# Kernel tuning notes

Hardware: AMD Instinct MI355X
Metric: run time of the kernel (lower is better)

## Reference

```python
import jax, jax.numpy as jnp
import numpy as np

N = 8192      # nodes
C = 128       # node_channels
E = 262144    # edges (avg degree 32)


def _glorot(key, shape):
    lim = 1.0 / np.sqrt(shape[0])
    return jax.random.uniform(key, shape, jnp.float32, -lim, lim)


def setup_inputs() -> dict:
    key = jax.random.key(0)
    ks = jax.random.split(key, 12)
    inp = {
        "x": jax.random.normal(ks[0], (N, C), jnp.float32),
        "edge_index": jax.random.randint(ks[1], (2, E), 0, N, dtype=jnp.int32).astype(jnp.int64),
        # edge encoder: two parallel GCNConv layers producing source/target embeddings
        "Ws": _glorot(ks[2], (C, C)), "bs": jnp.zeros((C,), jnp.float32),
        "Wt": _glorot(ks[3], (C, C)), "bt": jnp.zeros((C,), jnp.float32),
        # NodeModel GCNConv weights (layers used in forward: 1, 2, mu, 5, 6)
        "W1": _glorot(ks[4], (C, C)), "b1": jnp.zeros((C,), jnp.float32),
        "W2": _glorot(ks[5], (C, C)), "b2": jnp.zeros((C,), jnp.float32),
        "Wmu": _glorot(ks[6], (C, C)), "bmu": jnp.zeros((C,), jnp.float32),
        "W5": _glorot(ks[7], (C, C)), "b5": jnp.zeros((C,), jnp.float32),
        "W6": _glorot(ks[8], (C, C)), "b6": jnp.zeros((C,), jnp.float32),
    }
    return inp


def _gcn(x, W, b, src, dst, dis, n):
    """GCNConv: D^-1/2 (A + I) D^-1/2 X W + b, edge flow src -> dst."""
    h = x @ W                                    # [n, C]
    norm = dis[src] * dis[dst]                   # [E]
    agg = jax.ops.segment_sum(h[src] * norm[:, None], dst, num_segments=n)
    agg = agg + h * (dis * dis)[:, None]         # self-loop term
    return agg + b


def reference(x, edge_index, Ws, bs, Wt, bt, W1, b1, W2, b2, Wmu, bmu, W5, b5, W6, b6):
    src, dst = edge_index[0], edge_index[1]
    n = x.shape[0]
    # degree with self-loops (shared by all GCN layers, same graph)
    deg = jax.ops.segment_sum(jnp.ones((src.shape[0],), x.dtype), dst, num_segments=n) + 1.0
    dis = deg ** -0.5

    # edge encoder -> source/target embeddings, dense inner-product decoder (sigmoid=False)
    s = _gcn(x, Ws, bs, src, dst, dis, n)
    t = _gcn(x, Wt, bt, src, dst, dis, n)
    adj_pred = s @ t.T                           # [n, n]

    # NodeModel (eval mode: reparametrize returns mu; logstd branch is dead code)
    h = jax.nn.relu(_gcn(x, W1, b1, src, dst, dis, n))
    h = jax.nn.relu(_gcn(h, W2, b2, src, dst, dis, n))
    h = _gcn(h, Wmu, bmu, src, dst, dis, n)
    h = jax.nn.relu(_gcn(h, W5, b5, src, dst, dis, n))
    h = jax.nn.relu(_gcn(h, W6, b6, src, dst, dis, n))
    return adj_pred, h
```

## Files before the change

### kernel.cpp

```cpp
#include <hip/hip_runtime.h>
#include <hip/hip_bf16.h>

#define CCH 128

typedef __attribute__((ext_vector_type(8))) short s8v;
typedef __attribute__((ext_vector_type(4))) float f4v;

__device__ __forceinline__ unsigned short f2bf(float f){
  unsigned int u = __float_as_uint(f);
  u += 0x7fffu + ((u >> 16) & 1u);
  return (unsigned short)(u >> 16);
}

__global__ void k_deg(const int* __restrict__ dst, int* __restrict__ deg, int e){
  int i = blockIdx.x * blockDim.x + threadIdx.x;
  if (i < e) atomicAdd(&deg[dst[i]], 1);
}

__global__ __launch_bounds__(256) void k_disscale(const int* __restrict__ deg,
    const float* __restrict__ x, float* __restrict__ dis, float* __restrict__ g, int n){
  int t = blockIdx.x * 256 + threadIdx.x;
  int i = t >> 5, c = t & 31;
  if (i >= n) return;
  float di = rsqrtf((float)deg[i] + 1.0f);
  if (c == 0) dis[i] = di;
  float4 v = ((const float4*)x)[(size_t)i * 32 + c];
  v.x *= di; v.y *= di; v.z *= di; v.w *= di;
  ((float4*)g)[(size_t)i * 32 + c] = v;
}

__global__ void k_scan(const int* __restrict__ deg, int* __restrict__ row_ptr,
                       int* __restrict__ cursor, int n){
  __shared__ int part[1024];
  int t = threadIdx.x;
  int base = t * 8;
  int loc[8];
  int s = 0;
  #pragma unroll
  for (int i = 0; i < 8; ++i){ loc[i] = s; s += deg[base + i]; }
  part[t] = s;
  __syncthreads();
  for (int off = 1; off < 1024; off <<= 1){
    int v = (t >= off) ? part[t - off] : 0;
    __syncthreads();
    part[t] += v;
    __syncthreads();
  }
  int prev = t ? part[t - 1] : 0;
  #pragma unroll
  for (int i = 0; i < 8; ++i){
    int v = prev + loc[i];
    row_ptr[base + i] = v;
    cursor[base + i]  = v;
  }
  if (t == 0) row_ptr[n] = part[1023];
}

__global__ void k_scatter(const int* __restrict__ src, const int* __restrict__ dst,
                          int* __restrict__ cursor, int* __restrict__ csr_src, int e){
  int i = blockIdx.x * blockDim.x + threadIdx.x;
  if (i < e){
    int d = dst[i];
    int pos = atomicAdd(&cursor[d], 1);
    csr_src[pos] = src[i];
  }
}

__global__ __launch_bounds__(256) void k_agg(const float* __restrict__ g,
    const int* __restrict__ row_ptr, const int* __restrict__ csr_src,
    float* __restrict__ out, int n){
  int node = (blockIdx.x * blockDim.x + threadIdx.x) >> 6;
  int lane = threadIdx.x & 63;
  if (node >= n) return;
  node = __builtin_amdgcn_readfirstlane(node);
  const float2* g2 = (const float2*)g;
  int st = row_ptr[node], en = row_ptr[node + 1];
  float2 sv = g2[(size_t)node * 64 + lane];
  float ax0 = sv.x, ay0 = sv.y;
  float ax1 = 0.f, ay1 = 0.f, ax2 = 0.f, ay2 = 0.f, ax3 = 0.f, ay3 = 0.f;
  float ax4 = 0.f, ay4 = 0.f, ax5 = 0.f, ay5 = 0.f, ax6 = 0.f, ay6 = 0.f;
  float ax7 = 0.f, ay7 = 0.f;
  int e = st;
  for (; e + 8 <= en; e += 8){
    int s0 = csr_src[e + 0], s1 = csr_src[e + 1], s2 = csr_src[e + 2], s3 = csr_src[e + 3];
    int s4 = csr_src[e + 4], s5 = csr_src[e + 5], s6 = csr_src[e + 6], s7 = csr_src[e + 7];
    float2 v0 = g2[(size_t)s0 * 64 + lane];
    float2 v1 = g2[(size_t)s1 * 64 + lane];
    float2 v2 = g2[(size_t)s2 * 64 + lane];
    float2 v3 = g2[(size_t)s3 * 64 + lane];
    float2 v4 = g2[(size_t)s4 * 64 + lane];
    float2 v5 = g2[(size_t)s5 * 64 + lane];
    float2 v6 = g2[(size_t)s6 * 64 + lane];
    float2 v7 = g2[(size_t)s7 * 64 + lane];
    ax0 += v0.x; ay0 += v0.y;  ax1 += v1.x; ay1 += v1.y;
    ax2 += v2.x; ay2 += v2.y;  ax3 += v3.x; ay3 += v3.y;
    ax4 += v4.x; ay4 += v4.y;  ax5 += v5.x; ay5 += v5.y;
    ax6 += v6.x; ay6 += v6.y;  ax7 += v7.x; ay7 += v7.y;
  }
  for (; e < en; ++e){
    int s = csr_src[e];
    float2 v = g2[(size_t)s * 64 + lane];
    ax0 += v.x; ay0 += v.y;
  }
  float2 o;
  o.x = ((ax0 + ax1) + (ax2 + ax3)) + ((ax4 + ax5) + (ax6 + ax7));
  o.y = ((ay0 + ay1) + (ay2 + ay3)) + ((ay4 + ay5) + (ay6 + ay7));
  ((float2*)out)[(size_t)node * 64 + lane] = o;
}

__global__ __launch_bounds__(256) void k_gemm(const float* __restrict__ A,
    const float* __restrict__ W, const float* __restrict__ bias,
    const float* __restrict__ dis, float* __restrict__ out,
    int relu, int scale_out){
  __shared__ float sW[CCH * CCH];
  __shared__ float sA[16 * CCH];
  int tid = threadIdx.x;
  const float4* W4 = (const float4*)W;
  float4* sW4 = (float4*)sW;
  #pragma unroll
  for (int i = 0; i < 16; ++i) sW4[tid + i * 256] = W4[tid + i * 256];
  int row0 = blockIdx.x * 16;
  const float4* A4 = (const float4*)(A + (size_t)row0 * CCH);
  float4* sA4 = (float4*)sA;
  sA4[tid]       = A4[tid];
  sA4[tid + 256] = A4[tid + 256];
  __syncthreads();

  int r  = tid >> 4;
  int c0 = (tid & 15) << 3;
  float acc[8] = {0.f,0.f,0.f,0.f,0.f,0.f,0.f,0.f};
  #pragma unroll 4
  for (int k = 0; k < CCH; ++k){
    float a = sA[r * CCH + k];
    const float* wr = &sW[k * CCH + c0];
    #pragma unroll
    for (int j = 0; j < 8; ++j) acc[j] += a * wr[j];
  }
  float di = dis[row0 + r];
  size_t g0 = (size_t)(row0 + r) * CCH + c0;
  #pragma unroll
  for (int j = 0; j < 8; ++j){
    float v = fmaf(di, acc[j], bias[c0 + j]);
    if (relu) v = fmaxf(v, 0.f);
    if (scale_out) v *= di;
    out[g0 + j] = v;
  }
}

__global__ void k_tobf16(const float4* __restrict__ a, const float4* __restrict__ b,
                         ushort4* __restrict__ ao, ushort4* __restrict__ bo, int total4){
  int i = blockIdx.x * blockDim.x + threadIdx.x;
  if (i < total4){
    float4 va = a[i];
    float4 vb = b[i];
    ushort4 oa = { f2bf(va.x), f2bf(va.y), f2bf(va.z), f2bf(va.w) };
    ushort4 ob = { f2bf(vb.x), f2bf(vb.y), f2bf(vb.z), f2bf(vb.w) };
    ao[i] = oa;
    bo[i] = ob;
  }
}

__global__ __launch_bounds__(256) void k_adj(const unsigned short* __restrict__ S,
                                             const unsigned short* __restrict__ T,
                                             float* __restrict__ out, int n){
  __shared__ unsigned short sS[128 * 128];
  __shared__ unsigned short sT[128 * 128];
  int tid = threadIdx.x;
  int ntile = n >> 7;
  int tm = blockIdx.x / ntile;
  int tn = blockIdx.x % ntile;

  #pragma unroll
  for (int i = 0; i < 8; ++i){
    int cidx = i * 256 + tid;
    int row = cidx >> 4;
    int o   = cidx & 15;
    int boff = (o * 16) ^ ((row & 7) << 4);
    s8v v = ((const s8v*)(S + (size_t)(tm * 128 + row) * CCH))[o];
    *(s8v*)((char*)sS + row * 256 + boff) = v;
    s8v w = ((const s8v*)(T + (size_t)(tn * 128 + row) * CCH))[o];
    *(s8v*)((char*)sT + row * 256 + boff) = w;
  }
  __syncthreads();

  int lane = tid & 63;
  int w = tid >> 6;
  int wm = (w >> 1) * 64;
  int wn = (w & 1) * 64;

  f4v zero = {0.f, 0.f, 0.f, 0.f};
  f4v acc[4][4];
  #pragma unroll
  for (int a = 0; a < 4; ++a)
    #pragma unroll
    for (int b = 0; b < 4; ++b) acc[a][b] = zero;

  #pragma unroll
  for (int ks = 0; ks < 4; ++ks){
    int boff = ks * 64 + (lane >> 4) * 16;
    s8v af[4], bf[4];
    #pragma unroll
    for (int mi = 0; mi < 4; ++mi){
      int row = wm + mi * 16 + (lane & 15);
      af[mi] = *(const s8v*)((const char*)sS + row * 256 + (boff ^ ((row & 7) << 4)));
    }
    #pragma unroll
    for (int ni = 0; ni < 4; ++ni){
      int row = wn + ni * 16 + (lane & 15);
      bf[ni] = *(const s8v*)((const char*)sT + row * 256 + (boff ^ ((row & 7) << 4)));
    }
    #pragma unroll
    for (int mi = 0; mi < 4; ++mi)
      #pragma unroll
      for (int ni = 0; ni < 4; ++ni)
        acc[mi][ni] = __builtin_amdgcn_mfma_f32_16x16x32_bf16(af[mi], bf[ni], acc[mi][ni], 0, 0, 0);
  }

  int rbase = tm * 128 + wm + (lane >> 4) * 4;
  int cbase = tn * 128 + wn + (lane & 15);
  #pragma unroll
  for (int mi = 0; mi < 4; ++mi)
    #pragma unroll
    for (int ni = 0; ni < 4; ++ni){
      int rr = rbase + mi * 16;
      int cc = cbase + ni * 16;
      #pragma unroll
      for (int r = 0; r < 4; ++r)
        out[(size_t)(rr + r) * n + cc] = acc[mi][ni][r];
    }
}

extern "C" void kernel_launch(void* const* d_in, const int* in_sizes, int n_in,
                              void* d_out, int out_size, void* d_ws, size_t ws_size,
                              hipStream_t stream) {
  const float* x  = (const float*)d_in[0];
  const int*   ei = (const int*)d_in[1];
  const int n = in_sizes[0] / CCH;
  const int e = in_sizes[1] / 2;
  const int* srcv = ei;
  const int* dstv = ei + e;
  const float *Ws  = (const float*)d_in[2],  *bs  = (const float*)d_in[3];
  const float *Wt  = (const float*)d_in[4],  *bt  = (const float*)d_in[5];
  const float *W1  = (const float*)d_in[6],  *b1  = (const float*)d_in[7];
  const float *W2  = (const float*)d_in[8],  *b2  = (const float*)d_in[9];
  const float *Wmu = (const float*)d_in[10], *bmu = (const float*)d_in[11];
  const float *W5  = (const float*)d_in[12], *b5  = (const float*)d_in[13];
  const float *W6  = (const float*)d_in[14], *b6  = (const float*)d_in[15];

  char* ws = (char*)d_ws;
  size_t off = 0;
  auto alloc = [&](size_t bytes) -> void* {
    void* p = ws + off;
    off += (bytes + 255) & ~(size_t)255;
    return p;
  };
  int*   deg     = (int*)alloc((size_t)n * 4);
  float* dis     = (float*)alloc((size_t)n * 4);
  int*   row_ptr = (int*)alloc((size_t)(n + 1) * 4);
  int*   cursor  = (int*)alloc((size_t)n * 4);
  int*   csr_src = (int*)alloc((size_t)e * 4);
  float* g0      = (float*)alloc((size_t)n * CCH * 4);
  float* sumX    = (float*)alloc((size_t)n * CCH * 4);
  float* sbuf    = (float*)alloc((size_t)n * CCH * 4);
  float* tbuf    = (float*)alloc((size_t)n * CCH * 4);
  float* bufA    = (float*)alloc((size_t)n * CCH * 4);
  float* bufB    = (float*)alloc((size_t)n * CCH * 4);
  unsigned short* sb = (unsigned short*)alloc((size_t)n * CCH * 2);
  unsigned short* tb = (unsigned short*)alloc((size_t)n * CCH * 2);

  float* adj  = (float*)d_out;
  float* hout = (float*)d_out + (size_t)n * n;

  hipMemsetAsync(deg, 0, (size_t)n * 4, stream);
  k_deg     <<<(e + 255) / 256, 256, 0, stream>>>(dstv, deg, e);
  k_scan    <<<1, 1024, 0, stream>>>(deg, row_ptr, cursor, n);
  k_disscale<<<(n * 32) / 256, 256, 0, stream>>>(deg, x, dis, g0, n);
  k_scatter <<<(e + 255) / 256, 256, 0, stream>>>(srcv, dstv, cursor, csr_src, e);

  k_agg <<<n / 4, 256, 0, stream>>>(g0, row_ptr, csr_src, sumX, n);
  k_gemm<<<n / 16, 256, 0, stream>>>(sumX, Ws, bs, dis, sbuf, 0, 0);
  k_gemm<<<n / 16, 256, 0, stream>>>(sumX, Wt, bt, dis, tbuf, 0, 0);
  k_gemm<<<n / 16, 256, 0, stream>>>(sumX, W1, b1, dis, bufA, 1, 1);

  k_tobf16<<<((n * CCH / 4) + 255) / 256, 256, 0, stream>>>(
      (const float4*)sbuf, (const float4*)tbuf, (ushort4*)sb, (ushort4*)tb, n * CCH / 4);
  int nt = n / 128;
  k_adj<<<nt * nt, 256, 0, stream>>>(sb, tb, adj, n);

  k_agg <<<n / 4, 256, 0, stream>>>(bufA, row_ptr, csr_src, sumX, n);
  k_gemm<<<n / 16, 256, 0, stream>>>(sumX, W2, b2, dis, bufB, 1, 1);
  k_agg <<<n / 4, 256, 0, stream>>>(bufB, row_ptr, csr_src, sumX, n);
  k_gemm<<<n / 16, 256, 0, stream>>>(sumX, Wmu, bmu, dis, bufA, 0, 1);
  k_agg <<<n / 4, 256, 0, stream>>>(bufA, row_ptr, csr_src, sumX, n);
  k_gemm<<<n / 16, 256, 0, stream>>>(sumX, W5, b5, dis, bufB, 1, 1);
  k_agg <<<n / 4, 256, 0, stream>>>(bufB, row_ptr, csr_src, sumX, n);
  k_gemm<<<n / 16, 256, 0, stream>>>(sumX, W6, b6, dis, hout, 1, 0);
}
```

Baseline: 499.2 us.

## Use split-bf16 MFMA GEMMs, fuse multi-weight GEMM, co-schedule aggregation with adj

Replaces the scalar fp32 128x128 GEMM with an MFMA bf16 kernel that emulates fp32 precision via hi/lo split (three MFMAs per tile), with weights pre-split and transposed once. The aggregation kernel now emits hi/lo bf16 directly, and a single GEMM launch computes the S, T and layer-1 outputs, writing bf16 S/T and removing the separate conversion kernel. The dense adjacency tile kernel is merged with the next layer's aggregation into one launch so the gather work can fill idle CUs alongside the adj GEMM. It trades some precision (split bf16 drops lo*lo terms) and adds weight-split preprocessing.

```diff
diff --git a/kernel.cpp b/kernel.cpp
--- a/kernel.cpp
+++ b/kernel.cpp
@@ -2,6 +2,7 @@
 #include <hip/hip_bf16.h>
 
 #define CCH 128
+#define NADJ 4096
 
 typedef __attribute__((ext_vector_type(8))) short s8v;
 typedef __attribute__((ext_vector_type(4))) float f4v;
@@ -10,6 +11,9 @@
   unsigned int u = __float_as_uint(f);
   u += 0x7fffu + ((u >> 16) & 1u);
   return (unsigned short)(u >> 16);
+}
+__device__ __forceinline__ float bf2f(unsigned short h){
+  return __uint_as_float(((unsigned int)h) << 16);
 }
 
 __global__ void k_deg(const int* __restrict__ dst, int* __restrict__ deg, int e){
@@ -66,13 +70,36 @@
   }
 }
 
-__global__ __launch_bounds__(256) void k_agg(const float* __restrict__ g,
+__global__ __launch_bounds__(256) void k_wsplit(
+    const float* __restrict__ w0, const float* __restrict__ w1, const float* __restrict__ w2,
+    const float* __restrict__ w3, const float* __restrict__ w4, const float* __restrict__ w5,
+    const float* __restrict__ w6,
+    unsigned short* __restrict__ Wth, unsigned short* __restrict__ Wtl){
+  int l = blockIdx.x >> 2;
+  int seg = blockIdx.x & 3;
+  const float* W;
+  switch (l){
+    case 0: W = w0; break; case 1: W = w1; break; case 2: W = w2; break;
+    case 3: W = w3; break; case 4: W = w4; break; case 5: W = w5; break;
+    default: W = w6; break;
+  }
+  unsigned short* oh = Wth + (size_t)l * 16384;
+  unsigned short* ol = Wtl + (size_t)l * 16384;
+  #pragma unroll
+  for (int j = 0; j < 16; ++j){
+    int i = seg * 4096 + j * 256 + threadIdx.x;
+    int nn = i >> 7, kk = i & 127;
+    float v = W[kk * CCH + nn];
+    unsigned short h = f2bf(v);
+    unsigned short lo = f2bf(v - bf2f(h));
+    oh[i] = h;
+    ol[i] = lo;
+  }
+}
+
+__device__ __forceinline__ void agg_body(int node, int lane, const float* __restrict__ g,
     const int* __restrict__ row_ptr, const int* __restrict__ csr_src,
-    float* __restrict__ out, int n){
-  int node = (blockIdx.x * blockDim.x + threadIdx.x) >> 6;
-  int lane = threadIdx.x & 63;
-  if (node >= n) return;
-  node = __builtin_amdgcn_readfirstlane(node);
+    unsigned short* __restrict__ Ahi, unsigned short* __restrict__ Alo){
   const float2* g2 = (const float2*)g;
   int st = row_ptr[node], en = row_ptr[node + 1];
   float2 sv = g2[(size_t)node * 64 + lane];
@@ -102,67 +129,163 @@
     float2 v = g2[(size_t)s * 64 + lane];
     ax0 += v.x; ay0 += v.y;
   }
-  float2 o;
-  o.x = ((ax0 + ax1) + (ax2 + ax3)) + ((ax4 + ax5) + (ax6 + ax7));
-  o.y = ((ay0 + ay1) + (ay2 + ay3)) + ((ay4 + ay5) + (ay6 + ay7));
-  ((float2*)out)[(size_t)node * 64 + lane] = o;
-}
-
-__global__ __launch_bounds__(256) void k_gemm(const float* __restrict__ A,
-    const float* __restrict__ W, const float* __restrict__ bias,
-    const float* __restrict__ dis, float* __restrict__ out,
-    int relu, int scale_out){
-  __shared__ float sW[CCH * CCH];
-  __shared__ float sA[16 * CCH];
+  float ox = ((ax0 + ax1) + (ax2 + ax3)) + ((ax4 + ax5) + (ax6 + ax7));
+  float oy = ((ay0 + ay1) + (ay2 + ay3)) + ((ay4 + ay5) + (ay6 + ay7));
+  unsigned short hx = f2bf(ox);
+  unsigned short lx = f2bf(ox - bf2f(hx));
+  unsigned short hy = f2bf(oy);
+  unsigned short ly = f2bf(oy - bf2f(hy));
+  ushort2 hv, lv;
+  hv.x = hx; hv.y = hy;
+  lv.x = lx; lv.y = ly;
+  ((ushort2*)Ahi)[(size_t)node * 64 + lane] = hv;
+  ((ushort2*)Alo)[(size_t)node * 64 + lane] = lv;
+}
+
+__global__ __launch_bounds__(256) void k_agg(const float* __restrict__ g,
+    const int* __restrict__ row_ptr, const int* __restrict__ csr_src,
+    unsigned short* __restrict__ Ahi, unsigned short* __restrict__ Alo, int n){
+  int node = (blockIdx.x * blockDim.x + threadIdx.x) >> 6;
+  int lane = threadIdx.x & 63;
+  if (node >= n) return;
+  node = __builtin_amdgcn_readfirstlane(node);
+  agg_body(node, lane, g, row_ptr, csr_src, Ahi, Alo);
+}
+
+struct GemmArgs {
+  const unsigned short* wh[3];
+  const unsigned short* wl[3];
+  const float* bias[3];
+  void* out[3];
+  int mode[3];
+  int nw;
+};
+
+__global__ __launch_bounds__(256) void k_gemm(const unsigned short* __restrict__ Ahi,
+    const unsigned short* __restrict__ Alo, const float* __restrict__ dis, GemmArgs args){
+  __shared__ unsigned short sAh[32 * CCH];
+  __shared__ unsigned short sAl[32 * CCH];
+  __shared__ unsigned short sWh[CCH * CCH];
+  __shared__ unsigned short sWl[CCH * CCH];
   int tid = threadIdx.x;
-  const float4* W4 = (const float4*)W;
-  float4* sW4 = (float4*)sW;
-  #pragma unroll
-  for (int i = 0; i < 16; ++i) sW4[tid + i * 256] = W4[tid + i * 256];
-  int row0 = blockIdx.x * 16;
-  const float4* A4 = (const float4*)(A + (size_t)row0 * CCH);
-  float4* sA4 = (float4*)sA;
-  sA4[tid]       = A4[tid];
-  sA4[tid + 256] = A4[tid + 256];
+  int row0 = blockIdx.x * 32;
+
+  #pragma unroll
+  for (int j = 0; j < 2; ++j){
+    int c = j * 256 + tid;
+    int row = c >> 4, o = c & 15;
+    int boff = (o * 16) ^ ((row & 7) << 4);
+    *(s8v*)((char*)sAh + row * 256 + boff) = ((const s8v*)(Ahi + (size_t)(row0 + row) * CCH))[o];
+    *(s8v*)((char*)sAl + row * 256 + boff) = ((const s8v*)(Alo + (size_t)(row0 + row) * CCH))[o];
+  }
+  {
+    const unsigned short* wh = args.wh[0];
+    const unsigned short* wl = args.wl[0];
+    #pragma unroll
+    for (int j = 0; j < 8; ++j){
+      int c = j * 256 + tid;
+      int row = c >> 4, o = c & 15;
+      int boff = (o * 16) ^ ((row & 7) << 4);
+      *(s8v*)((char*)sWh + row * 256 + boff) = ((const s8v*)(wh + (size_t)row * CCH))[o];
+      *(s8v*)((char*)sWl + row * 256 + boff) = ((const s8v*)(wl + (size_t)row * CCH))[o];
+    }
+  }
   __syncthreads();
 
-  int r  = tid >> 4;
-  int c0 = (tid & 15) << 3;
-  float acc[8] = {0.f,0.f,0.f,0.f,0.f,0.f,0.f,0.f};
-  #pragma unroll 4
-  for (int k = 0; k < CCH; ++k){
-    float a = sA[r * CCH + k];
-    const float* wr = &sW[k * CCH + c0];
-    #pragma unroll
-    for (int j = 0; j < 8; ++j) acc[j] += a * wr[j];
-  }
-  float di = dis[row0 + r];
-  size_t g0 = (size_t)(row0 + r) * CCH + c0;
-  #pragma unroll
-  for (int j = 0; j < 8; ++j){
-    float v = fmaf(di, acc[j], bias[c0 + j]);
-    if (relu) v = fmaxf(v, 0.f);
-    if (scale_out) v *= di;
-    out[g0 + j] = v;
-  }
-}
-
-__global__ void k_tobf16(const float4* __restrict__ a, const float4* __restrict__ b,
-                         ushort4* __restrict__ ao, ushort4* __restrict__ bo, int total4){
-  int i = blockIdx.x * blockDim.x + threadIdx.x;
-  if (i < total4){
-    float4 va = a[i];
-    float4 vb = b[i];
-    ushort4 oa = { f2bf(va.x), f2bf(va.y), f2bf(va.z), f2bf(va.w) };
-    ushort4 ob = { f2bf(vb.x), f2bf(vb.y), f2bf(vb.z), f2bf(vb.w) };
-    ao[i] = oa;
-    bo[i] = ob;
-  }
-}
-
-__global__ __launch_bounds__(256) void k_adj(const unsigned short* __restrict__ S,
-                                             const unsigned short* __restrict__ T,
-                                             float* __restrict__ out, int n){
+  int lane = tid & 63;
+  int w = tid >> 6;
+
+  s8v ah[2][4], al[2][4];
+  #pragma unroll
+  for (int mi = 0; mi < 2; ++mi){
+    int row = mi * 16 + (lane & 15);
+    int sw = (row & 7) << 4;
+    #pragma unroll
+    for (int ks = 0; ks < 4; ++ks){
+      int boff = (ks * 64 + ((lane >> 4) * 16)) ^ sw;
+      ah[mi][ks] = *(const s8v*)((const char*)sAh + row * 256 + boff);
+      al[mi][ks] = *(const s8v*)((const char*)sAl + row * 256 + boff);
+    }
+  }
+
+  for (int l = 0; ; ++l){
+    f4v zero = {0.f, 0.f, 0.f, 0.f};
+    f4v acc[2][2];
+    acc[0][0] = zero; acc[0][1] = zero; acc[1][0] = zero; acc[1][1] = zero;
+
+    #pragma unroll
+    for (int ks = 0; ks < 4; ++ks){
+      s8v bh[2], bl[2];
+      #pragma unroll
+      for (int ni = 0; ni < 2; ++ni){
+        int row = w * 32 + ni * 16 + (lane & 15);
+        int boff = (ks * 64 + ((lane >> 4) * 16)) ^ ((row & 7) << 4);
+        bh[ni] = *(const s8v*)((const char*)sWh + row * 256 + boff);
+        bl[ni] = *(const s8v*)((const char*)sWl + row * 256 + boff);
+      }
+      #pragma unroll
+      for (int mi = 0; mi < 2; ++mi)
+        #pragma unroll
+        for (int ni = 0; ni < 2; ++ni){
+          acc[mi][ni] = __builtin_amdgcn_mfma_f32_16x16x32_bf16(ah[mi][ks], bh[ni], acc[mi][ni], 0, 0, 0);
+          acc[mi][ni] = __builtin_amdgcn_mfma_f32_16x16x32_bf16(ah[mi][ks], bl[ni], acc[mi][ni], 0, 0, 0);
+          acc[mi][ni] = __builtin_amdgcn_mfma_f32_16x16x32_bf16(al[mi][ks], bh[ni], acc[mi][ni], 0, 0, 0);
+        }
+    }
+
+    int mode = args.mode[l];
+    const float* bp = args.bias[l];
+    #pragma unroll
+    for (int mi = 0; mi < 2; ++mi){
+      f4v dv = ((const f4v*)(dis + row0 + mi * 16))[lane >> 4];
+      #pragma unroll
+      for (int ni = 0; ni < 2; ++ni){
+        int ccol = w * 32 + ni * 16 + (lane & 15);
+        float bv = bp[ccol];
+        #pragma unroll
+        for (int rr = 0; rr < 4; ++rr){
+          int rloc = mi * 16 + (lane >> 4) * 4 + rr;
+          float di = dv[rr];
+          float v = fmaf(di, acc[mi][ni][rr], bv);
+          if (mode & 1) v = fmaxf(v, 0.f);
+          if (mode & 2) v *= di;
+          size_t gidx = (size_t)(row0 + rloc) * CCH + ccol;
+          if (mode & 4) ((unsigned short*)args.out[l])[gidx] = f2bf(v);
+          else          ((float*)args.out[l])[gidx] = v;
+        }
+      }
+    }
+    if (l + 1 >= args.nw) break;
+    __syncthreads();
+    {
+      const unsigned short* wh = args.wh[l + 1];
+      const unsigned short* wl = args.wl[l + 1];
+      #pragma unroll
+      for (int j = 0; j < 8; ++j){
+        int c = j * 256 + tid;
+        int row = c >> 4, o = c & 15;
+        int boff = (o * 16) ^ ((row & 7) << 4);
+        *(s8v*)((char*)sWh + row * 256 + boff) = ((const s8v*)(wh + (size_t)row * CCH))[o];
+        *(s8v*)((char*)sWl + row * 256 + boff) = ((const s8v*)(wl + (size_t)row * CCH))[o];
+      }
+    }
+    __syncthreads();
+  }
+}
+
+__global__ __launch_bounds__(256) void k_adjagg(const unsigned short* __restrict__ S,
+    const unsigned short* __restrict__ T, float* __restrict__ out, int n,
+    const float* __restrict__ g, const int* __restrict__ row_ptr,
+    const int* __restrict__ csr_src, unsigned short* __restrict__ Ahi,
+    unsigned short* __restrict__ Alo){
+  if (blockIdx.x >= NADJ){
+    int node = ((blockIdx.x - NADJ) * 256 + threadIdx.x) >> 6;
+    int lane = threadIdx.x & 63;
+    if (node >= n) return;
+    node = __builtin_amdgcn_readfirstlane(node);
+    agg_body(node, lane, g, row_ptr, csr_src, Ahi, Alo);
+    return;
+  }
   __shared__ unsigned short sS[128 * 128];
   __shared__ unsigned short sT[128 * 128];
   int tid = threadIdx.x;
@@ -178,8 +301,8 @@
     int boff = (o * 16) ^ ((row & 7) << 4);
     s8v v = ((const s8v*)(S + (size_t)(tm * 128 + row) * CCH))[o];
     *(s8v*)((char*)sS + row * 256 + boff) = v;
-    s8v w = ((const s8v*)(T + (size_t)(tn * 128 + row) * CCH))[o];
-    *(s8v*)((char*)sT + row * 256 + boff) = w;
+    s8v w2 = ((const s8v*)(T + (size_t)(tn * 128 + row) * CCH))[o];
+    *(s8v*)((char*)sT + row * 256 + boff) = w2;
   }
   __syncthreads();
 
@@ -259,14 +382,13 @@
   int*   row_ptr = (int*)alloc((size_t)(n + 1) * 4);
   int*   cursor  = (int*)alloc((size_t)n * 4);
   int*   csr_src = (int*)alloc((size_t)e * 4);
-  float* g0      = (float*)alloc((size_t)n * CCH * 4);
-  float* sumX    = (float*)alloc((size_t)n * CCH * 4);
-  float* sbuf    = (float*)alloc((size_t)n * CCH * 4);
-  float* tbuf    = (float*)alloc((size_t)n * CCH * 4);
-  float* bufA    = (float*)alloc((size_t)n * CCH * 4);
-  float* bufB    = (float*)alloc((size_t)n * CCH * 4);
-  unsigned short* sb = (unsigned short*)alloc((size_t)n * CCH * 2);
-  unsigned short* tb = (unsigned short*)alloc((size_t)n * CCH * 2);
+  float* gbuf    = (float*)alloc((size_t)n * CCH * 4);
+  unsigned short* Ahi = (unsigned short*)alloc((size_t)n * CCH * 2);
+  unsigned short* Alo = (unsigned short*)alloc((size_t)n * CCH * 2);
+  unsigned short* sb  = (unsigned short*)alloc((size_t)n * CCH * 2);
+  unsigned short* tb  = (unsigned short*)alloc((size_t)n * CCH * 2);
+  unsigned short* Wth = (unsigned short*)alloc((size_t)7 * 16384 * 2);
+  unsigned short* Wtl = (unsigned short*)alloc((size_t)7 * 16384 * 2);
 
   float* adj  = (float*)d_out;
   float* hout = (float*)d_out + (size_t)n * n;
@@ -274,25 +396,37 @@
   hipMemsetAsync(deg, 0, (size_t)n * 4, stream);
   k_deg     <<<(e + 255) / 256, 256, 0, stream>>>(dstv, deg, e);
   k_scan    <<<1, 1024, 0, stream>>>(deg, row_ptr, cursor, n);
-  k_disscale<<<(n * 32) / 256, 256, 0, stream>>>(deg, x, dis, g0, n);
+  k_disscale<<<(n * 32) / 256, 256, 0, stream>>>(deg, x, dis, gbuf, n);
   k_scatter <<<(e + 255) / 256, 256, 0, stream>>>(srcv, dstv, cursor, csr_src, e);
-
-  k_agg <<<n / 4, 256, 0, stream>>>(g0, row_ptr, csr_src, sumX, n);
-  k_gemm<<<n / 16, 256, 0, stream>>>(sumX, Ws, bs, dis, sbuf, 0, 0);
-  k_gemm<<<n / 16, 256, 0, stream>>>(sumX, Wt, bt, dis, tbuf, 0, 0);
-  k_gemm<<<n / 16, 256, 0, stream>>>(sumX, W1, b1, dis, bufA, 1, 1);
-
-  k_tobf16<<<((n * CCH / 4) + 255) / 256, 256, 0, stream>>>(
-      (const float4*)sbuf, (const float4*)tbuf, (ushort4*)sb, (ushort4*)tb, n * CCH / 4);
-  int nt = n / 128;
-  k_adj<<<nt * nt, 256, 0, stream>>>(sb, tb, adj, n);
-
-  k_agg <<<n / 4, 256, 0, stream>>>(bufA, row_ptr, csr_src, sumX, n);
-  k_gemm<<<n / 16, 256, 0, stream>>>(sumX, W2, b2, dis, bufB, 1, 1);
-  k_agg <<<n / 4, 256, 0, stream>>>(bufB, row_ptr, csr_src, sumX, n);
-  k_gemm<<<n / 16, 256, 0, stream>>>(sumX, Wmu, bmu, dis, bufA, 0, 1);
-  k_agg <<<n / 4, 256, 0, stream>>>(bufA, row_ptr, csr_src, sumX, n);
-  k_gemm<<<n / 16, 256, 0, stream>>>(sumX, W5, b5, dis, bufB, 1, 1);
-  k_agg <<<n / 4, 256, 0, stream>>>(bufB, row_ptr, csr_src, sumX, n);
-  k_gemm<<<n / 16, 256, 0, stream>>>(sumX, W6, b6, dis, hout, 1, 0);
-}
+  k_wsplit  <<<28, 256, 0, stream>>>(Ws, Wt, W1, W2, Wmu, W5, W6, Wth, Wtl);
+
+  const unsigned short* wh[7]; const unsigned short* wl[7];
+  for (int i = 0; i < 7; ++i){ wh[i] = Wth + (size_t)i * 16384; wl[i] = Wtl + (size_t)i * 16384; }
+
+  k_agg<<<n / 4, 256, 0, stream>>>(gbuf, row_ptr, csr_src, Ahi, Alo, n);
+  {
+    GemmArgs a{};
+    a.wh[0] = wh[0]; a.wl[0] = wl[0]; a.bias[0] = bs; a.out[0] = sb;   a.mode[0] = 4;
+    a.wh[1] = wh[1]; a.wl[1] = wl[1]; a.bias[1] = bt; a.out[1] = tb;   a.mode[1] = 4;
+    a.wh[2] = wh[2]; a.wl[2] = wl[2]; a.bias[2] = b1; a.out[2] = gbuf; a.mode[2] = 3;
+    a.nw = 3;
+    k_gemm<<<n / 32, 256, 0, stream>>>(Ahi, Alo, dis, a);
+  }
+
+  k_adjagg<<<NADJ + n / 4, 256, 0, stream>>>(sb, tb, adj, n, gbuf, row_ptr, csr_src, Ahi, Alo);
+
+  auto gemm1 = [&](int wi, const float* bias, void* out, int mode){
+    GemmArgs a{};
+    a.wh[0] = wh[wi]; a.wl[0] = wl[wi]; a.bias[0] = bias; a.out[0] = out; a.mode[0] = mode;
+    a.nw = 1;
+    k_gemm<<<n / 32, 256, 0, stream>>>(Ahi, Alo, dis, a);
+  };
+
+  gemm1(3, b2, gbuf, 3);
+  k_agg<<<n / 4, 256, 0, stream>>>(gbuf, row_ptr, csr_src, Ahi, Alo, n);
+  gemm1(4, bmu, gbuf, 2);
+  k_agg<<<n / 4, 256, 0, stream>>>(gbuf, row_ptr, csr_src, Ahi, Alo, n);
+  gemm1(5, b5, gbuf, 3);
+  k_agg<<<n / 4, 256, 0, stream>>>(gbuf, row_ptr, csr_src, Ahi, Alo, n);
+  gemm1(6, b6, hout, 1);
+}
```

Result: faster. 462.2 us (-7.4%).
